# Kernel tuning notes

Measured on AMD Instinct MI355X. Metric: run time of the kernel, lower is better.

## Reference

```python
import jax, jax.numpy as jnp
import numpy as np
import math

DIM = 1024
D_IN = 2048      # expand * dim
N = 16           # d_state
NG = 32          # ngroups
DT_RANK = 64     # ceil(dim/16)
D_CONV = 4
B, L = 2, 1024


def setup_inputs() -> dict:
    key = jax.random.key(0)
    ks = jax.random.split(key, 10)
    nrm = lambda k, shp, s: jax.random.normal(k, shp, jnp.float32) * s
    x = jax.random.normal(ks[0], (B, L, DIM), jnp.float32)
    latent = jnp.zeros((B, NG, D_IN, N), jnp.float32)
    W_in = nrm(ks[1], (2 * D_IN, DIM), 0.02)          # in_proj (no bias)
    conv_w = nrm(ks[2], (D_IN, 1, D_CONV), 0.1)        # depthwise conv weight
    conv_b = nrm(ks[3], (D_IN,), 0.02)                 # conv bias
    W_x = nrm(ks[4], (DT_RANK + 2 * N, D_IN), 0.02)    # x_proj (no bias)
    W_dt = nrm(ks[5], (D_IN, DT_RANK), 0.02)           # dt_proj weight
    b_dt = nrm(ks[6], (D_IN,), 0.1)                    # dt_proj bias
    W_out = nrm(ks[7], (DIM, D_IN), 0.02)              # out_proj (no bias)
    A_log = jnp.log(jnp.tile(jnp.arange(1, N + 1, dtype=jnp.float32), (D_IN, 1)))
    D = jnp.ones((D_IN,), jnp.float32)
    W_cattn = nrm(ks[8], (3 * N, N), 0.02)             # c_attn (no bias)
    return dict(x=x, latent=latent, W_in=W_in, conv_w=conv_w, conv_b=conv_b,
                W_x=W_x, W_dt=W_dt, b_dt=b_dt, W_out=W_out, A_log=A_log,
                D=D, W_cattn=W_cattn)


def _scan_op(e1, e2):
    a1, b1 = e1
    a2, b2 = e2
    return a2 * a1, a2 * b1 + b2


def reference(x, latent, W_in, conv_w, conv_b, W_x, W_dt, b_dt, W_out, A_log, D, W_cattn):
    b, l, _ = x.shape
    xr = x @ W_in.T                                  # [b,l,2*d_in]
    u, res = xr[..., :D_IN], xr[..., D_IN:]
    # depthwise causal conv1d (padding d_conv-1 then truncate to l == left-pad)
    uc = jnp.transpose(u, (0, 2, 1))                 # [b,d_in,l]
    uc = jax.lax.conv_general_dilated(
        uc, conv_w, window_strides=(1,), padding=[(D_CONV - 1, 0)],
        feature_group_count=D_IN, dimension_numbers=('NCH', 'OIH', 'NCH'))
    uc = uc + conv_b[None, :, None]
    u = jax.nn.silu(jnp.transpose(uc, (0, 2, 1)))    # [b,l,d_in]

    A = -jnp.exp(A_log)                              # [d_in,n]
    x_dbl = u @ W_x.T                                # [b,l,dt_rank+2n]
    delta = jax.nn.softplus(x_dbl[..., :DT_RANK] @ W_dt.T + b_dt)  # [b,l,d_in]
    Bm = x_dbl[..., DT_RANK:DT_RANK + N]             # [b,l,n]
    Cm = x_dbl[..., DT_RANK + N:]                    # [b,l,n]

    dA = jnp.exp(delta[..., None] * A)               # [b,l,d_in,n]
    dBu = delta[..., None] * Bm[:, :, None, :] * u[..., None]  # [b,l,d_in,n]

    pg = l // NG
    dA = dA.reshape(b, NG, pg, D_IN, N)
    dBu = dBu.reshape(b, NG, pg, D_IN, N)
    Cg = Cm.reshape(b, NG, pg, N)
    dBu = dBu.at[:, :, 0].add(latent)                # inject group latent

    # parallel scan of h_t = dA_t * h_{t-1} + dBu_t within each group
    _, hs = jax.lax.associative_scan(_scan_op, (dA, dBu), axis=2)
    y = jnp.einsum('bgpdn,bgpn->bgpd', hs, Cg).reshape(b, l, D_IN)
    y = y + u * D

    # latent communication: causal attention over group latents (initial latent, per source)
    qkv = latent[:, :-1] @ W_cattn.T                 # [b,ng-1,d_in,3n]
    q, k, v = jnp.split(qkv, 3, axis=-1)
    G = NG - 1
    q = q.reshape(b, G, -1)
    k = k.reshape(b, G, -1)
    v = v.reshape(b, G, -1)
    scale = 1.0 / math.sqrt(D_IN * N)
    scores = (q @ jnp.swapaxes(k, 1, 2)) * scale     # [b,G,G]
    mask = jnp.tril(jnp.ones((G, G), bool))
    scores = jnp.where(mask, scores, -jnp.inf)
    attn = jax.nn.softmax(scores, axis=-1)
    lat = (attn @ v).reshape(b, G, D_IN, N)
    lat_out = jnp.concatenate([jnp.zeros((b, 1, D_IN, N), x.dtype), lat], axis=1)

    out = (y * jax.nn.silu(res)) @ W_out.T           # [b,l,dim]
    return out, lat_out
```

## Files before the change

kernel.cpp:

```cpp
#include <hip/hip_runtime.h>
#include <stdint.h>

typedef uint16_t u16;
typedef u16   u16x4  __attribute__((ext_vector_type(4)));
typedef u16   u16x8  __attribute__((ext_vector_type(8)));
typedef __bf16 bf16x8 __attribute__((ext_vector_type(8)));
typedef float f32x4  __attribute__((ext_vector_type(4)));

__device__ __forceinline__ float b2f(u16 x) {
    union { uint32_t u; float f; } c; c.u = ((uint32_t)x) << 16; return c.f;
}
__device__ __forceinline__ u16 f2b(float f) {
    union { float f; uint32_t u; } c; c.f = f;
    uint32_t r = c.u + 0x7FFFu + ((c.u >> 16) & 1u);
    return (u16)(r >> 16);
}
__device__ __forceinline__ float silu_f(float x) { return x / (1.f + __expf(-x)); }

__device__ __forceinline__ void gload16(const u16* g, u16* l) {
    __builtin_amdgcn_global_load_lds(
        (const __attribute__((address_space(1))) void*)(g),
        (__attribute__((address_space(3))) void*)(l), 16, 0, 0);
}

__device__ __forceinline__ int dtype_flag_block(const u16* __restrict__ xraw) {
    __shared__ int bad;
    if (threadIdx.x == 0) bad = 0;
    __syncthreads();
    float v = b2f(xraw[threadIdx.x]);
    if (!(fabsf(v) < 1000.f)) atomicAdd(&bad, 1);
    __syncthreads();
    return bad;
}

struct CvtArgs {
    const void* s[13];
    u16* d[13];
    int cum[14];
    int total;
};
__global__ __launch_bounds__(256) void cvt_all_k(CvtArgs a, const u16* __restrict__ xraw)
{
    int flag = dtype_flag_block(xraw);
    int u4 = blockIdx.x * 256 + threadIdx.x;
    if (u4 >= a.total) return;
    int seg = 0;
    while (u4 >= a.cum[seg + 1]) seg++;
    int local = u4 - a.cum[seg];
    const void* s = a.s[seg];
    u16x4 o;
    if (s == nullptr) {
        o[0] = o[1] = o[2] = o[3] = 0;
    } else if (flag) {
        f32x4 vv = ((const f32x4*)s)[local];
        for (int e = 0; e < 4; e++) o[e] = f2b(vv[e]);
    } else {
        o = ((const u16x4*)s)[local];
    }
    *(u16x4*)(a.d[seg] + (size_t)local * 4) = o;
}

template<int EPI>
__global__ __launch_bounds__(256) void gemm_bt(
    const u16* __restrict__ A, const u16* __restrict__ B,
    int Kc, int lda, int ldb,
    u16* __restrict__ Cb, float* __restrict__ Cf, int ldc, int ncols,
    const u16* __restrict__ bias, size_t zslab)
{
    __shared__ __align__(16) u16 lA[128 * 64];
    __shared__ __align__(16) u16 lB[128 * 64];
    const int tid  = threadIdx.x;
    const int wave = tid >> 6, lane = tid & 63;
    const int quad = lane >> 4, l16 = lane & 15;
    const int wm = wave & 1, wn = wave >> 1;
    const int row0 = blockIdx.y * 128, col0 = blockIdx.x * 128;
    const int kbeg = blockIdx.z * Kc;

    f32x4 acc[4][4];
    const f32x4 zf = {0.f, 0.f, 0.f, 0.f};
    for (int i = 0; i < 4; i++) for (int j = 0; j < 4; j++) acc[i][j] = zf;

    const u16* Ap[4]; const u16* Bp[4]; int lbase[4];
    for (int t = 0; t < 4; t++) {
        int c = t * 256 + tid;
        int r = c >> 3, s = c & 7;
        int q = (s - (r >> 1)) & 7;
        Ap[t] = A + (size_t)(row0 + r) * lda + q * 8 + kbeg;
        Bp[t] = B + (size_t)(col0 + r) * ldb + q * 8 + kbeg;
        lbase[t] = (t * 256 + wave * 64) * 8;
    }

    for (int k0 = 0; k0 < Kc; k0 += 64) {
        for (int t = 0; t < 4; t++) gload16(Ap[t] + k0, &lA[lbase[t]]);
        for (int t = 0; t < 4; t++) gload16(Bp[t] + k0, &lB[lbase[t]]);
        __syncthreads();
        for (int half = 0; half < 2; half++) {
            bf16x8 af[4], bfr[4];
            for (int i = 0; i < 4; i++) {
                int r = wm * 64 + i * 16 + l16;
                int s = (half * 4 + quad + (r >> 1)) & 7;
                af[i] = *(const bf16x8*)&lA[r * 64 + s * 8];
            }
            for (int j = 0; j < 4; j++) {
                int r = wn * 64 + j * 16 + l16;
                int s = (half * 4 + quad + (r >> 1)) & 7;
                bfr[j] = *(const bf16x8*)&lB[r * 64 + s * 8];
            }
            for (int i = 0; i < 4; i++)
                for (int j = 0; j < 4; j++)
                    acc[i][j] = __builtin_amdgcn_mfma_f32_16x16x32_bf16(af[i], bfr[j], acc[i][j], 0, 0, 0);
        }
        __syncthreads();
    }

    float* dstf = (EPI == 2) ? (Cf + (size_t)blockIdx.z * zslab) : Cf;
    for (int i = 0; i < 4; i++) {
        int mb = row0 + wm * 64 + i * 16 + quad * 4;
        for (int j = 0; j < 4; j++) {
            int n = col0 + wn * 64 + j * 16 + l16;
            if (n >= ncols) continue;
            if (EPI == 0) {
                for (int v = 0; v < 4; v++)
                    Cb[(size_t)(mb + v) * ldc + n] = f2b(acc[i][j][v]);
            } else if (EPI == 1) {
                float bv = b2f(bias[n]);
                for (int v = 0; v < 4; v++) {
                    float xx = acc[i][j][v] + bv;
                    dstf[(size_t)(mb + v) * ldc + n] =
                        fmaxf(xx, 0.f) + log1pf(__expf(-fabsf(xx)));
                }
            } else {
                for (int v = 0; v < 4; v++)
                    dstf[(size_t)(mb + v) * ldc + n] = acc[i][j][v];
            }
        }
    }
}

__global__ __launch_bounds__(256) void redc_k(
    const float* __restrict__ part, u16* __restrict__ dst,
    int KS, int NPAD, int ncols4, int M, int total)
{
    int gid = blockIdx.x * 256 + threadIdx.x;
    if (gid >= total) return;
    int m = gid / ncols4;
    int j = (gid - m * ncols4) * 4;
    f32x4 s = {0.f, 0.f, 0.f, 0.f};
    for (int ks = 0; ks < KS; ks++) {
        f32x4 p = *(const f32x4*)&part[((size_t)ks * M + m) * NPAD + j];
        for (int e = 0; e < 4; e++) s[e] += p[e];
    }
    u16x4 o;
    for (int e = 0; e < 4; e++) o[e] = f2b(s[e]);
    *(u16x4*)&dst[(size_t)m * (ncols4 * 4) + j] = o;
}

__global__ __launch_bounds__(256) void redout_k(
    const float* __restrict__ part, void* __restrict__ dout,
    const u16* __restrict__ xraw)
{
    int flag = dtype_flag_block(xraw);
    int gid = blockIdx.x * 256 + threadIdx.x;
    int m = gid >> 8;
    int j = (gid & 255) * 4;
    f32x4 s = {0.f, 0.f, 0.f, 0.f};
    for (int ks = 0; ks < 4; ks++) {
        f32x4 p = *(const f32x4*)&part[((size_t)ks * 2048 + m) * 1024 + j];
        for (int e = 0; e < 4; e++) s[e] += p[e];
    }
    for (int e = 0; e < 4; e++) if (!(fabsf(s[e]) < 1e30f)) s[e] = 0.f;
    if (flag) {
        ((f32x4*)dout)[(size_t)m * 256 + (j >> 2)] = s;
    } else {
        u16x4 o;
        for (int e = 0; e < 4; e++) o[e] = f2b(s[e]);
        ((u16x4*)dout)[(size_t)m * 256 + (j >> 2)] = o;
    }
}

__global__ __launch_bounds__(256) void conv_silu_k(
    const u16* __restrict__ xr, const u16* __restrict__ cw,
    const u16* __restrict__ cb, u16* __restrict__ u)
{
    int tid = threadIdx.x;
    int bl  = blockIdx.x;
    int l   = bl & 1023;
    int d0  = tid * 8;
    float acc[8];
    u16x8 bias = *(const u16x8*)&cb[d0];
    for (int j = 0; j < 8; j++) acc[j] = b2f(bias[j]);
    union { u16x8 v[4]; u16 s[32]; } wb;
    for (int t = 0; t < 4; t++) wb.v[t] = *(const u16x8*)&cw[d0 * 4 + t * 8];
    for (int t = 0; t < 4; t++) {
        int ls = l - 3 + t;
        if (ls < 0) continue;
        u16x8 xv = *(const u16x8*)&xr[(size_t)(bl - 3 + t) * 4096 + d0];
        for (int j = 0; j < 8; j++) acc[j] += b2f(xv[j]) * b2f(wb.s[j * 4 + t]);
    }
    u16x8 o;
    for (int j = 0; j < 8; j++) o[j] = f2b(silu_f(acc[j]));
    *(u16x8*)&u[(size_t)bl * 2048 + d0] = o;
}

__global__ __launch_bounds__(256) void scan_k(
    const float* __restrict__ delta, const u16* __restrict__ u,
    const u16* __restrict__ xr, const u16* __restrict__ xdbl,
    const u16* __restrict__ latent, const u16* __restrict__ Alog,
    const u16* __restrict__ Dp, u16* __restrict__ yg)
{
    int tid = threadIdx.x;
    int blk = blockIdx.x;
    int dblk = blk & 7, bg = blk >> 3;
    int d = dblk * 256 + tid;
    __shared__ float Bs[32][16], Cs[32][16];
    for (int idx = tid; idx < 512; idx += 256) {
        int p = idx >> 4, n = idx & 15;
        const u16* xp = &xdbl[(size_t)(bg * 32 + p) * 96];
        Bs[p][n] = b2f(xp[64 + n]);
        Cs[p][n] = b2f(xp[80 + n]);
    }
    __syncthreads();
    float a[16], h[16];
    {
        u16x8 a0 = *(const u16x8*)&Alog[(size_t)d * 16];
        u16x8 a1 = *(const u16x8*)&Alog[(size_t)d * 16 + 8];
        u16x8 l0 = *(const u16x8*)&latent[((size_t)bg * 2048 + d) * 16];
        u16x8 l1 = *(const u16x8*)&latent[((size_t)bg * 2048 + d) * 16 + 8];
        for (int n = 0; n < 8; n++) {
            a[n] = -__expf(b2f(a0[n])); a[8 + n] = -__expf(b2f(a1[n]));
            h[n] = b2f(l0[n]);          h[8 + n] = b2f(l1[n]);
        }
    }
    float Dd = b2f(Dp[d]);
    for (int p = 0; p < 32; p++) {
        size_t row = (size_t)bg * 32 + p;
        float dlt = delta[row * 2048 + d];
        float uu  = b2f(u[row * 2048 + d]);
        float db  = dlt * uu;
        float y = 0.f;
        if (p == 0) {
            for (int n = 0; n < 16; n++) { h[n] += db * Bs[0][n]; y += h[n] * Cs[0][n]; }
        } else {
            for (int n = 0; n < 16; n++) {
                float w = __expf(dlt * a[n]);
                h[n] = w * h[n] + db * Bs[p][n];
                y += h[n] * Cs[p][n];
            }
        }
        float rs = b2f(xr[row * 4096 + 2048 + d]);
        yg[row * 2048 + d] = f2b((y + uu * Dd) * silu_f(rs));
    }
}

__global__ __launch_bounds__(256) void qkv_k(
    const u16* __restrict__ latent, const u16* __restrict__ Wc,
    u16* __restrict__ q, u16* __restrict__ k, u16* __restrict__ v)
{
    __shared__ float Ws[48][16];
    for (int i = threadIdx.x; i < 768; i += 256) Ws[i >> 4][i & 15] = b2f(Wc[i]);
    __syncthreads();
    int gid = blockIdx.x * 256 + threadIdx.x;
    int d = gid & 2047;
    int bi = gid >> 11;
    int b = bi / 31, i = bi - b * 31;
    const u16* lp = &latent[(((size_t)b * 32 + i) * 2048 + d) * 16];
    float lv[16];
    {
        u16x8 l0 = *(const u16x8*)lp, l1 = *(const u16x8*)(lp + 8);
        for (int m = 0; m < 8; m++) { lv[m] = b2f(l0[m]); lv[8 + m] = b2f(l1[m]); }
    }
    u16* outs[3] = {q, k, v};
    for (int pl = 0; pl < 3; pl++) {
        u16x8 o0, o1;
        for (int n = 0; n < 16; n++) {
            float s = 0.f;
            for (int m = 0; m < 16; m++) s += lv[m] * Ws[pl * 16 + n][m];
            if (n < 8) o0[n] = f2b(s); else o1[n - 8] = f2b(s);
        }
        u16* op = outs[pl] + (size_t)bi * 32768 + d * 16;
        *(u16x8*)op = o0; *(u16x8*)(op + 8) = o1;
    }
}

__global__ __launch_bounds__(256) void scores_k(
    const u16* __restrict__ q, const u16* __restrict__ kk, float* __restrict__ sc)
{
    int idx = blockIdx.x;
    int b = idx / 961, r = idx - b * 961;
    int i = r / 31, j = r - i * 31;
    if (j > i) return;
    const u16* qp = q + ((size_t)b * 31 + i) * 32768;
    const u16* kp = kk + ((size_t)b * 31 + j) * 32768;
    float s = 0.f;
    for (int t = threadIdx.x * 8; t < 32768; t += 2048) {
        u16x8 a = *(const u16x8*)&qp[t];
        u16x8 c = *(const u16x8*)&kp[t];
        for (int e = 0; e < 8; e++) s += b2f(a[e]) * b2f(c[e]);
    }
    for (int off = 32; off; off >>= 1) s += __shfl_xor(s, off);
    __shared__ float red[4];
    if ((threadIdx.x & 63) == 0) red[threadIdx.x >> 6] = s;
    __syncthreads();
    if (threadIdx.x == 0)
        sc[idx] = (red[0] + red[1] + red[2] + red[3]) * 5.5242717e-3f;
}

__global__ __launch_bounds__(256) void attv_k(
    const float* __restrict__ sc, const u16* __restrict__ v,
    void* __restrict__ dout, const u16* __restrict__ xraw)
{
    int flag = dtype_flag_block(xraw);
    int blk = blockIdx.x;
    int chunk = blk & 15, bi = blk >> 4;
    int b = bi >> 5, i = (bi & 31) - 1;
    __shared__ float as[32];
    if (i >= 0 && threadIdx.x < 64) {
        float x = (threadIdx.x <= i) ? sc[(size_t)b * 961 + i * 31 + threadIdx.x] : -3.4e38f;
        float mx = x;
        for (int off = 32; off; off >>= 1) mx = fmaxf(mx, __shfl_xor(mx, off));
        float e = (threadIdx.x <= i) ? __expf(x - mx) : 0.f;
        float sm = e;
        for (int off = 32; off; off >>= 1) sm += __shfl_xor(sm, off);
        if (threadIdx.x < 32) as[threadIdx.x] = e / sm;
    }
    __syncthreads();
    int dn = chunk * 2048 + threadIdx.x * 8;
    float acc[8] = {0, 0, 0, 0, 0, 0, 0, 0};
    if (i >= 0) {
        for (int j = 0; j <= i; j++) {
            u16x8 vv = *(const u16x8*)&v[((size_t)b * 31 + j) * 32768 + dn];
            float aj = as[j];
            for (int e = 0; e < 8; e++) acc[e] += aj * b2f(vv[e]);
        }
        for (int e = 0; e < 8; e++) if (!(fabsf(acc[e]) < 1e30f)) acc[e] = 0.f;
    }
    size_t ofs = 2097152 + ((size_t)b * 32 + (i + 1)) * 32768 + dn;
    if (flag) {
        f32x4 o0, o1;
        for (int e = 0; e < 4; e++) { o0[e] = acc[e]; o1[e] = acc[4 + e]; }
        *(f32x4*)((float*)dout + ofs) = o0;
        *(f32x4*)((float*)dout + ofs + 4) = o1;
    } else {
        u16x8 o;
        for (int e = 0; e < 8; e++) o[e] = f2b(acc[e]);
        *(u16x8*)((u16*)dout + ofs) = o;
    }
}

extern "C" void kernel_launch(void* const* d_in, const int* in_sizes, int n_in,
                              void* d_out, int out_size, void* d_ws, size_t ws_size,
                              hipStream_t stream)
{
    char* ws = (char*)d_ws;
    const u16* xraw = (const u16*)d_in[0];
    u16* cx    = (u16*)(ws + 0);
    u16* clat  = (u16*)(ws + 4194304);
    u16* cWin  = (u16*)(ws + 8388608);
    u16* ccw   = (u16*)(ws + 16777216);
    u16* ccb   = (u16*)(ws + 16793600);
    u16* wxp   = (u16*)(ws + 16797696);
    u16* cWdt  = (u16*)(ws + 17321984);
    u16* cbdt  = (u16*)(ws + 17584128);
    u16* cWout = (u16*)(ws + 17588224);
    u16* cAlog = (u16*)(ws + 21782528);
    u16* cD    = (u16*)(ws + 21848064);
    u16* cWc   = (u16*)(ws + 21852160);
    u16*   xdbl      = (u16*)(ws + 21853760);
    float* sc        = (float*)(ws + 22246976);
    u16*   u         = (u16*)(ws + 22263360);
    u16*   xr        = (u16*)(ws + 30651968);
    u16*   yg        = (u16*)(ws + 47429184);
    float* delta     = (float*)(ws + 55817792);
    float* xdbl_part = (float*)(ws + 72595008);
    u16*   qb        = (u16*)(ws + 89372224);
    u16*   kb        = qb + 2031616;
    u16*   vb        = kb + 2031616;
    float* out_part  = (float*)(ws + 101561920);

    CvtArgs ca;
    const void* srcs[13] = { d_in[0], d_in[1], d_in[2], d_in[3], d_in[4],
                             d_in[5], nullptr, d_in[6], d_in[7], d_in[8],
                             d_in[9], d_in[10], d_in[11] };
    u16* dsts[13] = { cx, clat, cWin, ccw, ccb,
                      wxp, wxp + 196608, cWdt, cbdt, cWout,
                      cAlog, cD, cWc };
    int ns[13] = { 2097152, 2097152, 4194304, 8192, 2048,
                   196608, 65536, 131072, 2048, 2097152,
                   32768, 2048, 768 };
    int cum = 0;
    for (int i = 0; i < 13; i++) {
        ca.s[i] = srcs[i]; ca.d[i] = dsts[i];
        ca.cum[i] = cum; cum += ns[i] / 4;
    }
    ca.cum[13] = cum; ca.total = cum;
    cvt_all_k<<<(cum + 255) / 256, 256, 0, stream>>>(ca, xraw);

    gemm_bt<0><<<dim3(32, 16, 1), 256, 0, stream>>>(cx, cWin, 1024, 1024, 1024,
                                                    xr, nullptr, 4096, 4096, nullptr, 0);
    conv_silu_k<<<2048, 256, 0, stream>>>(xr, ccw, ccb, u);
    gemm_bt<2><<<dim3(1, 16, 16), 256, 0, stream>>>(u, wxp, 128, 2048, 2048,
                                                    nullptr, xdbl_part, 128, 128,
                                                    nullptr, (size_t)2048 * 128);
    redc_k<<<192, 256, 0, stream>>>(xdbl_part, xdbl, 16, 128, 24, 2048, 49152);
    gemm_bt<1><<<dim3(16, 16, 1), 256, 0, stream>>>(xdbl, cWdt, 64, 96, 64,
                                                    nullptr, delta, 2048, 2048, cbdt, 0);
    scan_k<<<512, 256, 0, stream>>>(delta, u, xr, xdbl, clat, cAlog, cD, yg);
    qkv_k<<<496, 256, 0, stream>>>(clat, cWc, qb, kb, vb);
    scores_k<<<1922, 256, 0, stream>>>(qb, kb, sc);
    attv_k<<<1024, 256, 0, stream>>>(sc, vb, d_out, xraw);
    gemm_bt<2><<<dim3(8, 16, 4), 256, 0, stream>>>(yg, cWout, 512, 2048, 2048,
                                                   nullptr, out_part, 1024, 1024,
                                                   nullptr, (size_t)2048 * 1024);
    redout_k<<<2048, 256, 0, stream>>>(out_part, d_out, xraw);
}
```

Before: 273.1 us.

## Fuse independent kernels into combined launches and use atomic split-K for x_proj

Replaces the x_proj split-K partial buffer and its reduction kernel with fp32 atomicAdd into a zeroed buffer, and has the dt_proj GEMM read that fp32 buffer directly, converting to bf16 while staging into LDS. The scan is merged with the latent qkv projection, the out_proj GEMM with the scores kernel, and the attention-value kernel with the output reduction, each by dispatching on block index. This cuts the number of launches and one reduction pass over memory. In exchange it adds atomic contention, nondeterministic summation order, and a synchronous fp32 load path in the dt GEMM.

```diff
diff --git a/kernel.cpp b/kernel.cpp
--- a/kernel.cpp
+++ b/kernel.cpp
@@ -34,9 +34,9 @@
 }
 
 struct CvtArgs {
-    const void* s[13];
-    u16* d[13];
-    int cum[14];
+    const void* s[14];
+    u16* d[14];
+    int cum[15];
     int total;
 };
 __global__ __launch_bounds__(256) void cvt_all_k(CvtArgs a, const u16* __restrict__ xraw)
@@ -60,9 +60,11 @@
     *(u16x4*)(a.d[seg] + (size_t)local * 4) = o;
 }
 
-template<int EPI>
-__global__ __launch_bounds__(256) void gemm_bt(
-    const u16* __restrict__ A, const u16* __restrict__ B,
+template<int EPI, int AF32>
+__device__ __forceinline__ void gemm_core(
+    int bx, int by, int bz,
+    const u16* __restrict__ Ab, const float* __restrict__ Af,
+    const u16* __restrict__ B,
     int Kc, int lda, int ldb,
     u16* __restrict__ Cb, float* __restrict__ Cf, int ldc, int ncols,
     const u16* __restrict__ bias, size_t zslab)
@@ -73,25 +75,39 @@
     const int wave = tid >> 6, lane = tid & 63;
     const int quad = lane >> 4, l16 = lane & 15;
     const int wm = wave & 1, wn = wave >> 1;
-    const int row0 = blockIdx.y * 128, col0 = blockIdx.x * 128;
-    const int kbeg = blockIdx.z * Kc;
+    const int row0 = by * 128, col0 = bx * 128;
+    const int kbeg = bz * Kc;
 
     f32x4 acc[4][4];
     const f32x4 zf = {0.f, 0.f, 0.f, 0.f};
     for (int i = 0; i < 4; i++) for (int j = 0; j < 4; j++) acc[i][j] = zf;
 
-    const u16* Ap[4]; const u16* Bp[4]; int lbase[4];
+    const u16* Abp[4]; const float* Afp[4]; const u16* Bp[4];
+    int lbase[4], lofsA[4];
     for (int t = 0; t < 4; t++) {
         int c = t * 256 + tid;
         int r = c >> 3, s = c & 7;
         int q = (s - (r >> 1)) & 7;
-        Ap[t] = A + (size_t)(row0 + r) * lda + q * 8 + kbeg;
+        if (AF32) Afp[t] = Af + (size_t)(row0 + r) * lda + q * 8 + kbeg;
+        else      Abp[t] = Ab + (size_t)(row0 + r) * lda + q * 8 + kbeg;
         Bp[t] = B + (size_t)(col0 + r) * ldb + q * 8 + kbeg;
         lbase[t] = (t * 256 + wave * 64) * 8;
+        lofsA[t] = c * 8;
     }
 
     for (int k0 = 0; k0 < Kc; k0 += 64) {
-        for (int t = 0; t < 4; t++) gload16(Ap[t] + k0, &lA[lbase[t]]);
+        if (AF32) {
+            for (int t = 0; t < 4; t++) {
+                const float* ap = Afp[t] + k0;
+                f32x4 v0 = *(const f32x4*)ap;
+                f32x4 v1 = *(const f32x4*)(ap + 4);
+                u16x8 w;
+                for (int e = 0; e < 4; e++) { w[e] = f2b(v0[e]); w[4 + e] = f2b(v1[e]); }
+                *(u16x8*)&lA[lofsA[t]] = w;
+            }
+        } else {
+            for (int t = 0; t < 4; t++) gload16(Abp[t] + k0, &lA[lbase[t]]);
+        }
         for (int t = 0; t < 4; t++) gload16(Bp[t] + k0, &lB[lbase[t]]);
         __syncthreads();
         for (int half = 0; half < 2; half++) {
@@ -113,7 +129,7 @@
         __syncthreads();
     }
 
-    float* dstf = (EPI == 2) ? (Cf + (size_t)blockIdx.z * zslab) : Cf;
+    float* dstf = (EPI == 2) ? (Cf + (size_t)bz * zslab) : Cf;
     for (int i = 0; i < 4; i++) {
         int mb = row0 + wm * 64 + i * 16 + quad * 4;
         for (int j = 0; j < 4; j++) {
@@ -129,53 +145,26 @@
                     dstf[(size_t)(mb + v) * ldc + n] =
                         fmaxf(xx, 0.f) + log1pf(__expf(-fabsf(xx)));
                 }
+            } else if (EPI == 2) {
+                for (int v = 0; v < 4; v++)
+                    dstf[(size_t)(mb + v) * ldc + n] = acc[i][j][v];
             } else {
                 for (int v = 0; v < 4; v++)
-                    dstf[(size_t)(mb + v) * ldc + n] = acc[i][j][v];
-            }
-        }
-    }
-}
-
-__global__ __launch_bounds__(256) void redc_k(
-    const float* __restrict__ part, u16* __restrict__ dst,
-    int KS, int NPAD, int ncols4, int M, int total)
-{
-    int gid = blockIdx.x * 256 + threadIdx.x;
-    if (gid >= total) return;
-    int m = gid / ncols4;
-    int j = (gid - m * ncols4) * 4;
-    f32x4 s = {0.f, 0.f, 0.f, 0.f};
-    for (int ks = 0; ks < KS; ks++) {
-        f32x4 p = *(const f32x4*)&part[((size_t)ks * M + m) * NPAD + j];
-        for (int e = 0; e < 4; e++) s[e] += p[e];
-    }
-    u16x4 o;
-    for (int e = 0; e < 4; e++) o[e] = f2b(s[e]);
-    *(u16x4*)&dst[(size_t)m * (ncols4 * 4) + j] = o;
-}
-
-__global__ __launch_bounds__(256) void redout_k(
-    const float* __restrict__ part, void* __restrict__ dout,
-    const u16* __restrict__ xraw)
-{
-    int flag = dtype_flag_block(xraw);
-    int gid = blockIdx.x * 256 + threadIdx.x;
-    int m = gid >> 8;
-    int j = (gid & 255) * 4;
-    f32x4 s = {0.f, 0.f, 0.f, 0.f};
-    for (int ks = 0; ks < 4; ks++) {
-        f32x4 p = *(const f32x4*)&part[((size_t)ks * 2048 + m) * 1024 + j];
-        for (int e = 0; e < 4; e++) s[e] += p[e];
-    }
-    for (int e = 0; e < 4; e++) if (!(fabsf(s[e]) < 1e30f)) s[e] = 0.f;
-    if (flag) {
-        ((f32x4*)dout)[(size_t)m * 256 + (j >> 2)] = s;
-    } else {
-        u16x4 o;
-        for (int e = 0; e < 4; e++) o[e] = f2b(s[e]);
-        ((u16x4*)dout)[(size_t)m * 256 + (j >> 2)] = o;
-    }
+                    atomicAdd(&dstf[(size_t)(mb + v) * ldc + n], acc[i][j][v]);
+            }
+        }
+    }
+}
+
+template<int EPI, int AF32>
+__global__ __launch_bounds__(256) void gemm_bt(
+    const u16* __restrict__ Ab, const float* __restrict__ Af,
+    const u16* __restrict__ B, int Kc, int lda, int ldb,
+    u16* __restrict__ Cb, float* __restrict__ Cf, int ldc, int ncols,
+    const u16* __restrict__ bias, size_t zslab)
+{
+    gemm_core<EPI, AF32>(blockIdx.x, blockIdx.y, blockIdx.z,
+                         Ab, Af, B, Kc, lda, ldb, Cb, Cf, ldc, ncols, bias, zslab);
 }
 
 __global__ __launch_bounds__(256) void conv_silu_k(
@@ -202,90 +191,99 @@
     *(u16x8*)&u[(size_t)bl * 2048 + d0] = o;
 }
 
-__global__ __launch_bounds__(256) void scan_k(
+__global__ __launch_bounds__(256) void scan_qkv_k(
     const float* __restrict__ delta, const u16* __restrict__ u,
-    const u16* __restrict__ xr, const u16* __restrict__ xdbl,
+    const u16* __restrict__ xr, const float* __restrict__ xf,
     const u16* __restrict__ latent, const u16* __restrict__ Alog,
-    const u16* __restrict__ Dp, u16* __restrict__ yg)
-{
+    const u16* __restrict__ Dp, u16* __restrict__ yg,
+    const u16* __restrict__ Wc, u16* __restrict__ q, u16* __restrict__ k,
+    u16* __restrict__ v)
+{
+    __shared__ float sm[1024];
     int tid = threadIdx.x;
-    int blk = blockIdx.x;
-    int dblk = blk & 7, bg = blk >> 3;
-    int d = dblk * 256 + tid;
-    __shared__ float Bs[32][16], Cs[32][16];
-    for (int idx = tid; idx < 512; idx += 256) {
-        int p = idx >> 4, n = idx & 15;
-        const u16* xp = &xdbl[(size_t)(bg * 32 + p) * 96];
-        Bs[p][n] = b2f(xp[64 + n]);
-        Cs[p][n] = b2f(xp[80 + n]);
-    }
-    __syncthreads();
-    float a[16], h[16];
-    {
-        u16x8 a0 = *(const u16x8*)&Alog[(size_t)d * 16];
-        u16x8 a1 = *(const u16x8*)&Alog[(size_t)d * 16 + 8];
-        u16x8 l0 = *(const u16x8*)&latent[((size_t)bg * 2048 + d) * 16];
-        u16x8 l1 = *(const u16x8*)&latent[((size_t)bg * 2048 + d) * 16 + 8];
-        for (int n = 0; n < 8; n++) {
-            a[n] = -__expf(b2f(a0[n])); a[8 + n] = -__expf(b2f(a1[n]));
-            h[n] = b2f(l0[n]);          h[8 + n] = b2f(l1[n]);
-        }
-    }
-    float Dd = b2f(Dp[d]);
-    for (int p = 0; p < 32; p++) {
-        size_t row = (size_t)bg * 32 + p;
-        float dlt = delta[row * 2048 + d];
-        float uu  = b2f(u[row * 2048 + d]);
-        float db  = dlt * uu;
-        float y = 0.f;
-        if (p == 0) {
-            for (int n = 0; n < 16; n++) { h[n] += db * Bs[0][n]; y += h[n] * Cs[0][n]; }
-        } else {
+    int bid = blockIdx.x;
+    if (bid < 512) {
+        float (*Bs)[16] = (float(*)[16])sm;
+        float (*Cs)[16] = (float(*)[16])(sm + 512);
+        int dblk = bid & 7, bg = bid >> 3;
+        int d = dblk * 256 + tid;
+        for (int idx = tid; idx < 512; idx += 256) {
+            int p = idx >> 4, n = idx & 15;
+            const float* xp = &xf[(size_t)(bg * 32 + p) * 128];
+            Bs[p][n] = xp[64 + n];
+            Cs[p][n] = xp[80 + n];
+        }
+        __syncthreads();
+        float a[16], h[16];
+        {
+            u16x8 a0 = *(const u16x8*)&Alog[(size_t)d * 16];
+            u16x8 a1 = *(const u16x8*)&Alog[(size_t)d * 16 + 8];
+            u16x8 l0 = *(const u16x8*)&latent[((size_t)bg * 2048 + d) * 16];
+            u16x8 l1 = *(const u16x8*)&latent[((size_t)bg * 2048 + d) * 16 + 8];
+            for (int n = 0; n < 8; n++) {
+                a[n] = -__expf(b2f(a0[n])); a[8 + n] = -__expf(b2f(a1[n]));
+                h[n] = b2f(l0[n]);          h[8 + n] = b2f(l1[n]);
+            }
+        }
+        float Dd = b2f(Dp[d]);
+        for (int p = 0; p < 32; p++) {
+            size_t row = (size_t)bg * 32 + p;
+            float dlt = delta[row * 2048 + d];
+            float uu  = b2f(u[row * 2048 + d]);
+            float db  = dlt * uu;
+            float y = 0.f;
+            if (p == 0) {
+                for (int n = 0; n < 16; n++) { h[n] += db * Bs[0][n]; y += h[n] * Cs[0][n]; }
+            } else {
+                for (int n = 0; n < 16; n++) {
+                    float w = __expf(dlt * a[n]);
+                    h[n] = w * h[n] + db * Bs[p][n];
+                    y += h[n] * Cs[p][n];
+                }
+            }
+            float rs = b2f(xr[row * 4096 + 2048 + d]);
+            yg[row * 2048 + d] = f2b((y + uu * Dd) * silu_f(rs));
+        }
+    } else {
+        float (*Ws)[16] = (float(*)[16])sm;
+        for (int i = tid; i < 768; i += 256) Ws[i >> 4][i & 15] = b2f(Wc[i]);
+        __syncthreads();
+        int gid = (bid - 512) * 256 + tid;
+        int d = gid & 2047;
+        int bi = gid >> 11;
+        int b = bi / 31, i = bi - b * 31;
+        const u16* lp = &latent[(((size_t)b * 32 + i) * 2048 + d) * 16];
+        float lv[16];
+        {
+            u16x8 l0 = *(const u16x8*)lp, l1 = *(const u16x8*)(lp + 8);
+            for (int m = 0; m < 8; m++) { lv[m] = b2f(l0[m]); lv[8 + m] = b2f(l1[m]); }
+        }
+        u16* outs[3] = {q, k, v};
+        for (int pl = 0; pl < 3; pl++) {
+            u16x8 o0, o1;
             for (int n = 0; n < 16; n++) {
-                float w = __expf(dlt * a[n]);
-                h[n] = w * h[n] + db * Bs[p][n];
-                y += h[n] * Cs[p][n];
-            }
-        }
-        float rs = b2f(xr[row * 4096 + 2048 + d]);
-        yg[row * 2048 + d] = f2b((y + uu * Dd) * silu_f(rs));
-    }
-}
-
-__global__ __launch_bounds__(256) void qkv_k(
-    const u16* __restrict__ latent, const u16* __restrict__ Wc,
-    u16* __restrict__ q, u16* __restrict__ k, u16* __restrict__ v)
-{
-    __shared__ float Ws[48][16];
-    for (int i = threadIdx.x; i < 768; i += 256) Ws[i >> 4][i & 15] = b2f(Wc[i]);
-    __syncthreads();
-    int gid = blockIdx.x * 256 + threadIdx.x;
-    int d = gid & 2047;
-    int bi = gid >> 11;
-    int b = bi / 31, i = bi - b * 31;
-    const u16* lp = &latent[(((size_t)b * 32 + i) * 2048 + d) * 16];
-    float lv[16];
-    {
-        u16x8 l0 = *(const u16x8*)lp, l1 = *(const u16x8*)(lp + 8);
-        for (int m = 0; m < 8; m++) { lv[m] = b2f(l0[m]); lv[8 + m] = b2f(l1[m]); }
-    }
-    u16* outs[3] = {q, k, v};
-    for (int pl = 0; pl < 3; pl++) {
-        u16x8 o0, o1;
-        for (int n = 0; n < 16; n++) {
-            float s = 0.f;
-            for (int m = 0; m < 16; m++) s += lv[m] * Ws[pl * 16 + n][m];
-            if (n < 8) o0[n] = f2b(s); else o1[n - 8] = f2b(s);
-        }
-        u16* op = outs[pl] + (size_t)bi * 32768 + d * 16;
-        *(u16x8*)op = o0; *(u16x8*)(op + 8) = o1;
-    }
-}
-
-__global__ __launch_bounds__(256) void scores_k(
+                float s = 0.f;
+                for (int m = 0; m < 16; m++) s += lv[m] * Ws[pl * 16 + n][m];
+                if (n < 8) o0[n] = f2b(s); else o1[n - 8] = f2b(s);
+            }
+            u16* op = outs[pl] + (size_t)bi * 32768 + d * 16;
+            *(u16x8*)op = o0; *(u16x8*)(op + 8) = o1;
+        }
+    }
+}
+
+__global__ __launch_bounds__(256) void gemm_scores_k(
+    const u16* __restrict__ yg, const u16* __restrict__ Wout, float* __restrict__ out_part,
     const u16* __restrict__ q, const u16* __restrict__ kk, float* __restrict__ sc)
 {
-    int idx = blockIdx.x;
+    int bid = blockIdx.x;
+    if (bid < 512) {
+        int bx = bid & 7, by = (bid >> 3) & 15, bz = bid >> 7;
+        gemm_core<2, 0>(bx, by, bz, yg, nullptr, Wout, 512, 2048, 2048,
+                        nullptr, out_part, 1024, 1024, nullptr, (size_t)2048 * 1024);
+        return;
+    }
+    int idx = bid - 512;
     int b = idx / 961, r = idx - b * 961;
     int i = r / 31, j = r - i * 31;
     if (j > i) return;
@@ -305,45 +303,65 @@
         sc[idx] = (red[0] + red[1] + red[2] + red[3]) * 5.5242717e-3f;
 }
 
-__global__ __launch_bounds__(256) void attv_k(
+__global__ __launch_bounds__(256) void attv_redout_k(
     const float* __restrict__ sc, const u16* __restrict__ v,
-    void* __restrict__ dout, const u16* __restrict__ xraw)
+    const float* __restrict__ part, void* __restrict__ dout,
+    const u16* __restrict__ xraw)
 {
     int flag = dtype_flag_block(xraw);
-    int blk = blockIdx.x;
-    int chunk = blk & 15, bi = blk >> 4;
-    int b = bi >> 5, i = (bi & 31) - 1;
-    __shared__ float as[32];
-    if (i >= 0 && threadIdx.x < 64) {
-        float x = (threadIdx.x <= i) ? sc[(size_t)b * 961 + i * 31 + threadIdx.x] : -3.4e38f;
-        float mx = x;
-        for (int off = 32; off; off >>= 1) mx = fmaxf(mx, __shfl_xor(mx, off));
-        float e = (threadIdx.x <= i) ? __expf(x - mx) : 0.f;
-        float sm = e;
-        for (int off = 32; off; off >>= 1) sm += __shfl_xor(sm, off);
-        if (threadIdx.x < 32) as[threadIdx.x] = e / sm;
-    }
-    __syncthreads();
-    int dn = chunk * 2048 + threadIdx.x * 8;
-    float acc[8] = {0, 0, 0, 0, 0, 0, 0, 0};
-    if (i >= 0) {
-        for (int j = 0; j <= i; j++) {
-            u16x8 vv = *(const u16x8*)&v[((size_t)b * 31 + j) * 32768 + dn];
-            float aj = as[j];
-            for (int e = 0; e < 8; e++) acc[e] += aj * b2f(vv[e]);
-        }
-        for (int e = 0; e < 8; e++) if (!(fabsf(acc[e]) < 1e30f)) acc[e] = 0.f;
-    }
-    size_t ofs = 2097152 + ((size_t)b * 32 + (i + 1)) * 32768 + dn;
-    if (flag) {
-        f32x4 o0, o1;
-        for (int e = 0; e < 4; e++) { o0[e] = acc[e]; o1[e] = acc[4 + e]; }
-        *(f32x4*)((float*)dout + ofs) = o0;
-        *(f32x4*)((float*)dout + ofs + 4) = o1;
+    int bid = blockIdx.x;
+    if (bid < 1024) {
+        int chunk = bid & 15, bi = bid >> 4;
+        int b = bi >> 5, i = (bi & 31) - 1;
+        __shared__ float as[32];
+        if (i >= 0 && threadIdx.x < 64) {
+            float x = (threadIdx.x <= i) ? sc[(size_t)b * 961 + i * 31 + threadIdx.x] : -3.4e38f;
+            float mx = x;
+            for (int off = 32; off; off >>= 1) mx = fmaxf(mx, __shfl_xor(mx, off));
+            float e = (threadIdx.x <= i) ? __expf(x - mx) : 0.f;
+            float sm = e;
+            for (int off = 32; off; off >>= 1) sm += __shfl_xor(sm, off);
+            if (threadIdx.x < 32) as[threadIdx.x] = e / sm;
+        }
+        __syncthreads();
+        int dn = chunk * 2048 + threadIdx.x * 8;
+        float acc[8] = {0, 0, 0, 0, 0, 0, 0, 0};
+        if (i >= 0) {
+            for (int j = 0; j <= i; j++) {
+                u16x8 vv = *(const u16x8*)&v[((size_t)b * 31 + j) * 32768 + dn];
+                float aj = as[j];
+                for (int e = 0; e < 8; e++) acc[e] += aj * b2f(vv[e]);
+            }
+            for (int e = 0; e < 8; e++) if (!(fabsf(acc[e]) < 1e30f)) acc[e] = 0.f;
+        }
+        size_t ofs = 2097152 + ((size_t)b * 32 + (i + 1)) * 32768 + dn;
+        if (flag) {
+            f32x4 o0, o1;
+            for (int e = 0; e < 4; e++) { o0[e] = acc[e]; o1[e] = acc[4 + e]; }
+            *(f32x4*)((float*)dout + ofs) = o0;
+            *(f32x4*)((float*)dout + ofs + 4) = o1;
+        } else {
+            u16x8 o;
+            for (int e = 0; e < 8; e++) o[e] = f2b(acc[e]);
+            *(u16x8*)((u16*)dout + ofs) = o;
+        }
     } else {
-        u16x8 o;
-        for (int e = 0; e < 8; e++) o[e] = f2b(acc[e]);
-        *(u16x8*)((u16*)dout + ofs) = o;
+        int gid = (bid - 1024) * 256 + threadIdx.x;
+        int m = gid >> 8;
+        int j = (gid & 255) * 4;
+        f32x4 s = {0.f, 0.f, 0.f, 0.f};
+        for (int ks = 0; ks < 4; ks++) {
+            f32x4 p = *(const f32x4*)&part[((size_t)ks * 2048 + m) * 1024 + j];
+            for (int e = 0; e < 4; e++) s[e] += p[e];
+        }
+        for (int e = 0; e < 4; e++) if (!(fabsf(s[e]) < 1e30f)) s[e] = 0.f;
+        if (flag) {
+            ((f32x4*)dout)[(size_t)m * 256 + (j >> 2)] = s;
+        } else {
+            u16x4 o;
+            for (int e = 0; e < 4; e++) o[e] = f2b(s[e]);
+            ((u16x4*)dout)[(size_t)m * 256 + (j >> 2)] = o;
+        }
     }
 }
 
@@ -365,51 +383,44 @@
     u16* cAlog = (u16*)(ws + 21782528);
     u16* cD    = (u16*)(ws + 21848064);
     u16* cWc   = (u16*)(ws + 21852160);
-    u16*   xdbl      = (u16*)(ws + 21853760);
-    float* sc        = (float*)(ws + 22246976);
-    u16*   u         = (u16*)(ws + 22263360);
-    u16*   xr        = (u16*)(ws + 30651968);
-    u16*   yg        = (u16*)(ws + 47429184);
-    float* delta     = (float*)(ws + 55817792);
-    float* xdbl_part = (float*)(ws + 72595008);
-    u16*   qb        = (u16*)(ws + 89372224);
-    u16*   kb        = qb + 2031616;
-    u16*   vb        = kb + 2031616;
-    float* out_part  = (float*)(ws + 101561920);
+    float* xdbl_f32 = (float*)(ws + 21853760);
+    float* sc       = (float*)(ws + 22902336);
+    u16*   u        = (u16*)(ws + 22910080);
+    u16*   xr       = (u16*)(ws + 31298688);
+    u16*   yg       = (u16*)(ws + 48075904);
+    float* delta    = (float*)(ws + 56464512);
+    u16*   qb       = (u16*)(ws + 73241728);
+    u16*   kb       = qb + 2031616;
+    u16*   vb       = kb + 2031616;
+    float* out_part = (float*)(ws + 85431424);
 
     CvtArgs ca;
-    const void* srcs[13] = { d_in[0], d_in[1], d_in[2], d_in[3], d_in[4],
+    const void* srcs[14] = { d_in[0], d_in[1], d_in[2], d_in[3], d_in[4],
                              d_in[5], nullptr, d_in[6], d_in[7], d_in[8],
-                             d_in[9], d_in[10], d_in[11] };
-    u16* dsts[13] = { cx, clat, cWin, ccw, ccb,
+                             d_in[9], d_in[10], d_in[11], nullptr };
+    u16* dsts[14] = { cx, clat, cWin, ccw, ccb,
                       wxp, wxp + 196608, cWdt, cbdt, cWout,
-                      cAlog, cD, cWc };
-    int ns[13] = { 2097152, 2097152, 4194304, 8192, 2048,
+                      cAlog, cD, cWc, (u16*)xdbl_f32 };
+    int ns[14] = { 2097152, 2097152, 4194304, 8192, 2048,
                    196608, 65536, 131072, 2048, 2097152,
-                   32768, 2048, 768 };
+                   32768, 2048, 768, 524288 };
     int cum = 0;
-    for (int i = 0; i < 13; i++) {
+    for (int i = 0; i < 14; i++) {
         ca.s[i] = srcs[i]; ca.d[i] = dsts[i];
         ca.cum[i] = cum; cum += ns[i] / 4;
     }
-    ca.cum[13] = cum; ca.total = cum;
+    ca.cum[14] = cum; ca.total = cum;
     cvt_all_k<<<(cum + 255) / 256, 256, 0, stream>>>(ca, xraw);
 
-    gemm_bt<0><<<dim3(32, 16, 1), 256, 0, stream>>>(cx, cWin, 1024, 1024, 1024,
-                                                    xr, nullptr, 4096, 4096, nullptr, 0);
+    gemm_bt<0, 0><<<dim3(32, 16, 1), 256, 0, stream>>>(cx, nullptr, cWin, 1024, 1024, 1024,
+                                                       xr, nullptr, 4096, 4096, nullptr, 0);
     conv_silu_k<<<2048, 256, 0, stream>>>(xr, ccw, ccb, u);
-    gemm_bt<2><<<dim3(1, 16, 16), 256, 0, stream>>>(u, wxp, 128, 2048, 2048,
-                                                    nullptr, xdbl_part, 128, 128,
-                                                    nullptr, (size_t)2048 * 128);
-    redc_k<<<192, 256, 0, stream>>>(xdbl_part, xdbl, 16, 128, 24, 2048, 49152);
-    gemm_bt<1><<<dim3(16, 16, 1), 256, 0, stream>>>(xdbl, cWdt, 64, 96, 64,
-                                                    nullptr, delta, 2048, 2048, cbdt, 0);
-    scan_k<<<512, 256, 0, stream>>>(delta, u, xr, xdbl, clat, cAlog, cD, yg);
-    qkv_k<<<496, 256, 0, stream>>>(clat, cWc, qb, kb, vb);
-    scores_k<<<1922, 256, 0, stream>>>(qb, kb, sc);
-    attv_k<<<1024, 256, 0, stream>>>(sc, vb, d_out, xraw);
-    gemm_bt<2><<<dim3(8, 16, 4), 256, 0, stream>>>(yg, cWout, 512, 2048, 2048,
-                                                   nullptr, out_part, 1024, 1024,
-                                                   nullptr, (size_t)2048 * 1024);
-    redout_k<<<2048, 256, 0, stream>>>(out_part, d_out, xraw);
-}
+    gemm_bt<3, 0><<<dim3(1, 16, 16), 256, 0, stream>>>(u, nullptr, wxp, 128, 2048, 2048,
+                                                       nullptr, xdbl_f32, 128, 128, nullptr, 0);
+    gemm_bt<1, 1><<<dim3(16, 16, 1), 256, 0, stream>>>(nullptr, xdbl_f32, cWdt, 64, 128, 64,
+                                                       nullptr, delta, 2048, 2048, cbdt, 0);
+    scan_qkv_k<<<1008, 256, 0, stream>>>(delta, u, xr, xdbl_f32, clat, cAlog, cD, yg,
+                                         cWc, qb, kb, vb);
+    gemm_scores_k<<<2434, 256, 0, stream>>>(yg, cWout, out_part, qb, kb, sc);
+    attv_redout_k<<<3072, 256, 0, stream>>>(sc, vb, out_part, d_out, xraw);
+}
```

After: 261.4 us. 4.3% less time.
